# Kernel tuning notes

Measured on AMD Instinct MI355X. Metric: run time of the kernel, lower is better.

Reference implementation:

```python
import jax, jax.numpy as jnp
import numpy as np

# ---- config (mirrors init_kwargs) ----
H = 128
W = 128
FMO_STEPS = 4
INPUT_FRAMES = 1
N_PIECES = 1
N_TERMS = 2
CAM_DIST = 2.0
ROT_DIVIDE = 1.0
SIGMAINV = 7000.0
ERODE_K = 5
FOCAL = float(1.0 / np.tan(1.57 / 4.0))  # generate_perspective_projection(1.57/2), aspect=1


def quaternion_to_angle_axis(q):
    # q: [B,4] in (w,x,y,z) convention (torchgeometry)
    q1, q2, q3 = q[..., 1], q[..., 2], q[..., 3]
    sin_sq = q1 * q1 + q2 * q2 + q3 * q3
    sin_t = jnp.sqrt(sin_sq + 1e-20)
    cos_t = q[..., 0]
    two_theta = 2.0 * jnp.where(cos_t < 0.0, jnp.arctan2(-sin_t, -cos_t), jnp.arctan2(sin_t, cos_t))
    k = jnp.where(sin_sq > 1e-12, two_theta / sin_t, 2.0)
    return q[..., 1:4] * k[..., None]


def angle_axis_to_rotation_matrix(aa):
    # aa: [B,3] -> [B,3,3] (Rodrigues)
    th = jnp.sqrt(jnp.sum(aa * aa, axis=-1, keepdims=True) + 1e-12)  # [B,1]
    k = aa / th
    kx, ky, kz = k[..., 0], k[..., 1], k[..., 2]
    zero = jnp.zeros_like(kx)
    K = jnp.stack([jnp.stack([zero, -kz, ky], -1),
                   jnp.stack([kz, zero, -kx], -1),
                   jnp.stack([-ky, kx, zero], -1)], -2)
    s = jnp.sin(th)[..., None]
    c = jnp.cos(th)[..., None]
    return jnp.eye(3, dtype=aa.dtype) + s * K + (1.0 - c) * jnp.matmul(K, K)


def rasterize(fv_img, fv_z, face_feat, fn_z):
    # fv_img [B,F,3,2] NDC, fv_z [B,F,3] camera z, face_feat [B,F,3,C], fn_z [B,F]
    B, F = fv_img.shape[:2]
    xs = jnp.linspace(-1.0, 1.0, W)
    ys = jnp.linspace(1.0, -1.0, H)
    py, px = jnp.meshgrid(ys, xs, indexing='ij')  # [H,W]
    a, b, c = fv_img[:, :, 0], fv_img[:, :, 1], fv_img[:, :, 2]  # [B,F,2]
    e0 = b - a
    e1 = c - a
    denom = e0[..., 0] * e1[..., 1] - e0[..., 1] * e1[..., 0]  # [B,F]
    valid = (fn_z > 0.0) & (jnp.abs(denom) > 1e-10)
    inv_den = jnp.where(jnp.abs(denom) > 1e-10, 1.0 / denom, 0.0)
    dx = px[None, None] - a[..., 0][..., None, None]  # [B,F,H,W]
    dy = py[None, None] - a[..., 1][..., None, None]
    w1 = (dx * e1[..., 1][..., None, None] - dy * e1[..., 0][..., None, None]) * inv_den[..., None, None]
    w2 = (e0[..., 0][..., None, None] * dy - e0[..., 1][..., None, None] * dx) * inv_den[..., None, None]
    w0 = 1.0 - w1 - w2
    inside = (w0 >= 0.0) & (w1 >= 0.0) & (w2 >= 0.0) & valid[..., None, None]
    zi = (w0 * fv_z[:, :, 0, None, None] + w1 * fv_z[:, :, 1, None, None] + w2 * fv_z[:, :, 2, None, None])
    score = jnp.where(inside, zi, -1e10)  # camera looks down -z: nearest face has max z
    best = jnp.argmax(score, axis=1)      # [B,H,W] z-buffer winner
    hit = jnp.any(inside, axis=1)
    bary = jnp.stack([w0, w1, w2], axis=-1)  # [B,F,H,W,3]
    idx = jnp.broadcast_to(best[:, None, :, :, None], (B, 1, H, W, 3))
    bary_b = jnp.take_along_axis(bary, idx, axis=1)[:, 0]  # [B,H,W,3]
    feat_b = jax.vmap(lambda f, i: f[i])(face_feat, best)  # [B,H,W,3,C]
    feats = jnp.einsum('bhwkc,bhwk->bhwc', feat_b, bary_b) * hit[..., None]
    # DIB-R soft silhouette: A = 1 - prod(1 - exp(-sigmainv*d^2)), d = dist to triangle, 0 inside
    d2 = None
    tri = (a, b, c)
    for i in range(3):
        p, q = tri[i], tri[(i + 1) % 3]
        ex = (q - p)[..., 0][..., None, None]
        ey = (q - p)[..., 1][..., None, None]
        rx = px[None, None] - p[..., 0][..., None, None]
        ry = py[None, None] - p[..., 1][..., None, None]
        L2 = ex * ex + ey * ey + 1e-12
        t = jnp.clip((rx * ex + ry * ey) / L2, 0.0, 1.0)
        dxe = rx - t * ex
        dye = ry - t * ey
        dd = dxe * dxe + dye * dye
        d2 = dd if d2 is None else jnp.minimum(d2, dd)
    d2 = jnp.where(inside, 0.0, d2)
    prob = jnp.where(valid[..., None, None], jnp.exp(-SIGMAINV * d2), 0.0)
    mask = 1.0 - jnp.prod(1.0 - prob, axis=1)  # [B,H,W]
    return feats, mask


def texture_sample(tex, uv):
    # tex [B,3,Th,Tw], uv [B,H,W,2] in [0,1]; bilinear, v axis flipped (image row 0 <-> v=1)
    Th, Tw = tex.shape[2], tex.shape[3]
    u = jnp.clip(uv[..., 0], 0.0, 1.0) * (Tw - 1)
    v = (1.0 - jnp.clip(uv[..., 1], 0.0, 1.0)) * (Th - 1)
    x0 = jnp.floor(u)
    y0 = jnp.floor(v)
    fx = (u - x0)[:, None]  # [B,1,H,W]
    fy = (v - y0)[:, None]
    x0i = jnp.clip(x0.astype(jnp.int32), 0, Tw - 1)
    x1i = jnp.clip(x0i + 1, 0, Tw - 1)
    y0i = jnp.clip(y0.astype(jnp.int32), 0, Th - 1)
    y1i = jnp.clip(y0i + 1, 0, Th - 1)
    g = jax.vmap(lambda t, yy, xx: t[:, yy, xx])  # [B,3,H,W]
    t00 = g(tex, y0i, x0i)
    t01 = g(tex, y0i, x1i)
    t10 = g(tex, y1i, x0i)
    t11 = g(tex, y1i, x1i)
    return t00 * (1 - fx) * (1 - fy) + t01 * fx * (1 - fy) + t10 * (1 - fx) * fy + t11 * fx * fy


def erode(m, k):
    # kornia erosion with an all-ones kxk kernel == min-pool (geodesic border)
    return -jax.lax.reduce_window(-m, -jnp.inf, jax.lax.max, (1, k, k), (1, 1, 1), 'SAME')


def render_frame(verts_world, faces, face_features, texture_maps):
    # camera at (0,0,CAM_DIST) looking at origin with up=(0,1,0): R_cam == I
    v_cam = verts_world - jnp.array([0.0, 0.0, CAM_DIST], dtype=verts_world.dtype)
    fv_cam = v_cam[:, faces]  # [B,F,3,3]
    n = jnp.cross(fv_cam[:, :, 1] - fv_cam[:, :, 0], fv_cam[:, :, 2] - fv_cam[:, :, 0])
    n = n / (jnp.linalg.norm(n, axis=-1, keepdims=True) + 1e-10)
    fn_z = n[..., 2]
    z = fv_cam[..., 2]  # negative in front of camera
    img = FOCAL * fv_cam[..., :2] / (-z[..., None] + 1e-10)  # [B,F,3,2]
    uv, mask = rasterize(img, z, face_features, fn_z)
    rgb = texture_sample(texture_maps, uv)  # [B,3,H,W]
    mask_e = erode(mask, ERODE_K)
    return jnp.concatenate([rgb, mask_e[:, None]], axis=1)  # [B,4,H,W]


def reference(vertices, translation, quaternion, exp, face_features, texture_maps, faces):
    rot = angle_axis_to_rotation_matrix(quaternion_to_angle_axis(quaternion[:, 0, 0]))
    trans_start = translation[:, :, 0, 0]  # [B,1,3]
    all_renders = []
    renders = []
    frames = 0
    time_before = 0.0
    for pind in range(N_PIECES):
        angles = quaternion_to_angle_axis(quaternion[:, pind, 1]) / ROT_DIVIDE
        rot_step = angle_axis_to_rotation_matrix(exp * angles / FMO_STEPS)
        rot_noexp = angle_axis_to_rotation_matrix(angles * (1.0 - exp))
        n_steps = FMO_STEPS * INPUT_FRAMES // N_PIECES  # prop[pind] (forced for single piece)
        for ti in np.linspace(0.0, 1.0, n_steps):
            if frames == 0:
                time_before = ti
            time_exp = time_before + (ti - time_before) * exp  # [1]
            verts = jnp.einsum('bij,bvj->bvi', rot, vertices) + trans_start
            for p in range(1, N_TERMS):
                verts = verts + (time_exp ** p) * translation[:, :, pind, p]
            renders.append(render_frame(verts, faces, face_features, texture_maps))
            frames += 1
            if frames == FMO_STEPS:
                frames = 0
                all_renders.append(jnp.stack(renders, 1))
                renders = []
                rot = jnp.matmul(rot, rot_noexp)
            else:
                rot = jnp.matmul(rot, rot_step)
        for p in range(1, N_TERMS):
            trans_start = trans_start + translation[:, :, pind, p]
    return jnp.stack(all_renders, 1)  # [B, input_frames, fmo_steps, 4, H, W]


def setup_inputs() -> dict:
    key = jax.random.key(0)
    ks = jax.random.split(key, 7)
    B, V, F = 1, 162, 320
    vertices = jax.random.normal(ks[0], (B, V, 3), jnp.float32) * 0.3
    translation = jax.random.normal(ks[1], (B, 1, N_PIECES, N_TERMS, 3), jnp.float32) * 0.1
    quaternion = jax.random.normal(ks[2], (B, N_PIECES, 2, 4), jnp.float32)
    exp = jax.random.uniform(ks[3], (1,), jnp.float32)
    face_features = jax.random.uniform(ks[4], (B, F, 3, 2), jnp.float32)
    texture_maps = jax.random.uniform(ks[5], (B, 3, 256, 256), jnp.float32)
    faces = jax.random.randint(ks[6], (F, 3), 0, V)
    return {"vertices": vertices, "translation": translation, "quaternion": quaternion,
            "exp": exp, "face_features": face_features, "texture_maps": texture_maps,
            "faces": faces}
```

## Files before the change

### kernel.cpp

```cpp
#include <hip/hip_runtime.h>
#include <math.h>

#define N_FRAMES 4
#define N_FACES  320
#define N_VERTS  162
#define IMG_H    128
#define IMG_W    128
#define NWAVES   8
#define FPW      40
#define REC_SZ   20

#define SV_OFF   0
#define BB_OFF   1952
#define BB_LD    48
#define REC_OFF  8096
#define ARENA_SZ 33696



__device__ __forceinline__ void q_to_aa(const float* q, float* aa) {
    float q1 = q[1], q2 = q[2], q3 = q[3];
    float sin_sq = (q1 * q1 + q2 * q2) + q3 * q3;
    float sin_t = sqrtf(sin_sq + 1e-20f);
    float cos_t = q[0];
    float two_theta = (cos_t < 0.0f) ? (2.0f * atan2f(-sin_t, -cos_t))
                                     : (2.0f * atan2f(sin_t, cos_t));
    float k = (sin_sq > 1e-12f) ? (two_theta / sin_t) : 2.0f;
    aa[0] = q1 * k; aa[1] = q2 * k; aa[2] = q3 * k;
}

__device__ __forceinline__ void aa_to_R(const float* aa, float* R) {
    float th = sqrtf(((aa[0] * aa[0] + aa[1] * aa[1]) + aa[2] * aa[2]) + 1e-12f);
    float kx = aa[0] / th, ky = aa[1] / th, kz = aa[2] / th;
    float K[9] = { 0.0f, -kz,  ky,
                   kz,  0.0f, -kx,
                  -ky,   kx, 0.0f };
    float s = sinf(th), c = cosf(th);
    float KK[9];
    for (int i = 0; i < 3; ++i)
        for (int j = 0; j < 3; ++j)
            KK[i*3+j] = (K[i*3+0] * K[0*3+j] + K[i*3+1] * K[1*3+j]) + K[i*3+2] * K[2*3+j];
    float omc = 1.0f - c;
    for (int i = 0; i < 9; ++i) {
        float eye = (i == 0 || i == 4 || i == 8) ? 1.0f : 0.0f;
        R[i] = (eye + s * K[i]) + omc * KK[i];
    }
}

__device__ __forceinline__ void mat3mul(const float* A, const float* B, float* C) {
    for (int i = 0; i < 3; ++i)
        for (int j = 0; j < 3; ++j)
            C[i*3+j] = (A[i*3+0] * B[0*3+j] + A[i*3+1] * B[1*3+j]) + A[i*3+2] * B[2*3+j];
}


__global__ void __launch_bounds__(512)
render_kernel(const float* __restrict__ verts_in,
              const float* __restrict__ transl,
              const float* __restrict__ quat,
              const float* __restrict__ expv,
              const int*   __restrict__ faces,
              const float* __restrict__ ffeat,
              const float* __restrict__ tex,
              float* __restrict__ out,
              float* __restrict__ maskbuf)
{
    __shared__ __align__(16) char arena[ARENA_SZ];
    __shared__ float rotS[9];
    float* sv   = (float*)(arena + SV_OFF);
    float* bb   = (float*)(arena + BB_OFF);
    float* recs = (float*)(arena + REC_OFF);
    float* red  = (float*)arena;

    int frame = blockIdx.x >> 8;
    int blk   = blockIdx.x & 255;
    int tid   = threadIdx.x;
    int lane  = tid & 63;
    int wv    = __builtin_amdgcn_readfirstlane(tid >> 6);
    int tile_x = blk & 7, tile_y = blk >> 3;
    int j = tile_x * 16 + (lane & 15);
    int i = tile_y * 4 + (lane >> 4);

    float e = expv[0];

    if (tid == 0) {
        float aa0[3], aa1[3], Rl[9], S[9];
        q_to_aa(quat, aa0);
        aa_to_R(aa0, Rl);
        q_to_aa(quat + 4, aa1);
        float arg[3];
        for (int t = 0; t < 3; ++t) arg[t] = (e * aa1[t]) / 4.0f;
        aa_to_R(arg, S);
        for (int t = 0; t < frame; ++t) {
            float nxt[9];
            mat3mul(Rl, S, nxt);
            for (int q = 0; q < 9; ++q) Rl[q] = nxt[q];
        }
        for (int q = 0; q < 9; ++q) rotS[q] = Rl[q];
    }
    __syncthreads();

    if (tid < N_VERTS) {
        float te = (float)((double)frame / 3.0) * e;
        float vx = verts_in[tid*3+0], vy = verts_in[tid*3+1], vz = verts_in[tid*3+2];
        float dx_ = (rotS[0] * vx + rotS[1] * vy) + rotS[2] * vz;
        float dy_ = (rotS[3] * vx + rotS[4] * vy) + rotS[5] * vz;
        float dz_ = (rotS[6] * vx + rotS[7] * vy) + rotS[8] * vz;
        float x = (dx_ + transl[0]) + te * transl[3];
        float y = (dy_ + transl[1]) + te * transl[4];
        float z = (dz_ + transl[2]) + te * transl[5];
        z = z - 2.0f;
        sv[tid*3+0] = x; sv[tid*3+1] = y; sv[tid*3+2] = z;
    }
    __syncthreads();

    const float FOCAL = (float)(1.0 / tan(1.57 / 4.0));
    int cnt;
    {
        bool valid = false;
        float ax=0, ay=0, bx=0, by=0, cx=0, cy=0, e0x=0, e0y=0, e1x=0, e1y=0;
        float e12x=0, e12y=0, z0=0, z1=0, z2=0, den=0;
        int f = wv * FPW + lane;
        if (lane < FPW) {
            int i0 = faces[f*3+0], i1 = faces[f*3+1], i2 = faces[f*3+2];
            const float* A = &sv[i0*3];
            const float* B = &sv[i1*3];
            const float* C = &sv[i2*3];
            float ux = B[0] - A[0], uy = B[1] - A[1];
            float wx = C[0] - A[0], wy = C[1] - A[1];
            float nz = ux * wy - uy * wx;
            float da = -A[2] + 1e-10f, db = -B[2] + 1e-10f, dc = -C[2] + 1e-10f;
            ax = (FOCAL * A[0]) / da; ay = (FOCAL * A[1]) / da;
            bx = (FOCAL * B[0]) / db; by = (FOCAL * B[1]) / db;
            cx = (FOCAL * C[0]) / dc; cy = (FOCAL * C[1]) / dc;
            e0x = bx - ax; e0y = by - ay;
            e1x = cx - ax; e1y = cy - ay;
            e12x = cx - bx; e12y = cy - by;
            den = e0x * e1y - e0y * e1x;
            z0 = A[2]; z1 = B[2]; z2 = C[2];
            valid = (fabsf(den) > 1e-10f) && (nz > 0.0f);
        }
        unsigned long long m = __ballot(valid);
        cnt = __popcll(m);
        if (valid) {
            unsigned long long lmask = (lane == 63) ? 0x7fffffffffffffffull
                                                    : ((1ull << lane) - 1ull);
            int pos = __popcll(m & lmask);
            float invden = 1.0f / den;
            float L2_0 = (e0x * e0x + e0y * e0y) + 1e-12f;
            float L2_1 = (e12x * e12x + e12y * e12y) + 1e-12f;
            float L2_2 = (e1x * e1x + e1y * e1y) + 1e-12f;
            float4* r = (float4*)&recs[(wv * FPW + pos) * REC_SZ];
            r[0] = make_float4(ax, ay, e0x, e0y);
            r[1] = make_float4(e1x, e1y, invden, (float)f);
            r[2] = make_float4(z0, z1, z2, 1.0f / L2_0);
            r[3] = make_float4(bx, by, e12x, e12y);
            r[4] = make_float4(cx, cy, 1.0f / L2_1, 1.0f / L2_2);
            float* wbb = &bb[wv * 4 * BB_LD];
            wbb[0*BB_LD + pos] = fminf(fminf(ax, bx), cx);
            wbb[1*BB_LD + pos] = fminf(fminf(ay, by), cy);
            wbb[2*BB_LD + pos] = fmaxf(fmaxf(ax, bx), cx);
            wbb[3*BB_LD + pos] = fmaxf(fmaxf(ay, by), cy);
        }
    }

    float px = (float)(-1.0 + 2.0 * (double)j / 127.0);
    float py = (float)( 1.0 - 2.0 * (double)i / 127.0);
    float txmin = (float)(-1.0 + 2.0 * (double)(tile_x * 16) / 127.0);
    float txmax = (float)(-1.0 + 2.0 * (double)(tile_x * 16 + 15) / 127.0);
    float tymax = (float)( 1.0 - 2.0 * (double)(tile_y * 4) / 127.0);
    float tymin = (float)( 1.0 - 2.0 * (double)(tile_y * 4 + 3) / 127.0);

    unsigned long long fmask;
    {
        int l = (lane < FPW) ? lane : 0;
        const float* wbb = &bb[wv * 4 * BB_LD];
        float xmin = wbb[0*BB_LD + l], ymin = wbb[1*BB_LD + l];
        float xmax = wbb[2*BB_LD + l], ymax = wbb[3*BB_LD + l];
        float cdx = fmaxf(fmaxf(xmin - txmax, txmin - xmax), 0.0f);
        float cdy = fmaxf(fmaxf(ymin - tymax, tymin - ymax), 0.0f);
        bool near = ((cdx * cdx + cdy * cdy) <= 0.0026f) && (lane < cnt);
        fmask = __ballot(near);
    }

    float best = -1e10f;
    int bestf = 0;
    float bw0 = 0.0f, bw1 = 0.0f, bw2 = 0.0f;
    float P = 1.0f;
    bool pzero = false;

    while (fmask) {
        int fc = __ffsll((unsigned long long)fmask) - 1;
        fmask &= fmask - 1;
        const float* d = &recs[(wv * FPW + fc) * REC_SZ];

        float ax = d[0], ay = d[1], e0x = d[2], e0y = d[3];
        float e1x = d[4], e1y = d[5], invden = d[6], fidx = d[7];
        float z0 = d[8], z1 = d[9], z2 = d[10];

        float dx = px - ax, dy = py - ay;
        float w1 = (dx * e1y - dy * e1x) * invden;
        float w2 = (e0x * dy - e0y * dx) * invden;
        float w0 = (1.0f - w1) - w2;
        bool inside = (w0 >= 0.0f) & (w1 >= 0.0f) & (w2 >= 0.0f);
        float zi = (w0 * z0 + w1 * z1) + w2 * z2;
        float score = inside ? zi : -1e10f;
        if (score > best) {
            best = score; bestf = (int)fidx; bw0 = w0; bw1 = w1; bw2 = w2;
        }

        if (!pzero) {
            float invL2_0 = d[11];
            float bx = d[12], by = d[13], e12x = d[14], e12y = d[15];
            float cx = d[16], cy = d[17], invL2_1 = d[18], invL2_2 = d[19];
            float t0 = fminf(fmaxf((dx * e0x + dy * e0y) * invL2_0, 0.0f), 1.0f);
            float x0 = dx - t0 * e0x, y0 = dy - t0 * e0y;
            float dd = x0 * x0 + y0 * y0;
            float rx1 = px - bx, ry1 = py - by;
            float t1 = fminf(fmaxf((rx1 * e12x + ry1 * e12y) * invL2_1, 0.0f), 1.0f);
            float x1 = rx1 - t1 * e12x, y1 = ry1 - t1 * e12y;
            dd = fminf(dd, x1 * x1 + y1 * y1);
            float ex2 = -e1x, ey2 = -e1y;
            float rx2 = px - cx, ry2 = py - cy;
            float t2 = fminf(fmaxf((rx2 * ex2 + ry2 * ey2) * invL2_2, 0.0f), 1.0f);
            float x2 = rx2 - t2 * ex2, y2 = ry2 - t2 * ey2;
            dd = fminf(dd, x2 * x2 + y2 * y2);

            float d2 = inside ? 0.0f : dd;
            float prob = __expf(-7000.0f * d2);
            P *= (1.0f - prob);
            pzero = __all(P == 0.0f);
        }
    }

    __syncthreads();
    float* my = &red[tid * 6];
    my[0] = best; my[1] = __int_as_float(bestf);
    my[2] = bw0;  my[3] = bw1; my[4] = bw2; my[5] = P;
    __syncthreads();

    if (tid < 64) {
        float bbst = red[tid * 6 + 0];
        int   bf   = __float_as_int(red[tid * 6 + 1]);
        float r0 = red[tid * 6 + 2], r1 = red[tid * 6 + 3], r2 = red[tid * 6 + 4];
        float Pt = red[tid * 6 + 5];
        for (int w = 1; w < NWAVES; ++w) {
            const float* s = &red[(w * 64 + tid) * 6];
            float sc = s[0]; int ff = __float_as_int(s[1]);
            if ((sc > bbst) || ((sc == bbst) && (ff < bf))) {
                bbst = sc; bf = ff; r0 = s[2]; r1 = s[3]; r2 = s[4];
            }
            Pt *= s[5];
        }

        bool hit = bbst != -1e10f;
        float uv0 = 0.0f, uv1 = 0.0f;
        if (hit) {
            const float* fp = ffeat + bf * 6;
            uv0 = (fp[0] * r0 + fp[2] * r1) + fp[4] * r2;
            uv1 = (fp[1] * r0 + fp[3] * r1) + fp[5] * r2;
        }
        float u = fminf(fmaxf(uv0, 0.0f), 1.0f) * 255.0f;
        float v = (1.0f - fminf(fmaxf(uv1, 0.0f), 1.0f)) * 255.0f;
        float x0f = floorf(u), y0f = floorf(v);
        float fx = u - x0f, fy = v - y0f;
        int x0i = min(max((int)x0f, 0), 255);
        int x1i = min(x0i + 1, 255);
        int y0i = min(max((int)y0f, 0), 255);
        int y1i = min(y0i + 1, 255);

        for (int c = 0; c < 3; ++c) {
            const float* tc = tex + c * 65536;
            float t00 = tc[y0i * 256 + x0i];
            float t01 = tc[y0i * 256 + x1i];
            float t10 = tc[y1i * 256 + x0i];
            float t11 = tc[y1i * 256 + x1i];
            float val = (t00 * (1.0f - fx)) * (1.0f - fy);
            val = val + (t01 * fx) * (1.0f - fy);
            val = val + (t10 * (1.0f - fx)) * fy;
            val = val + (t11 * fx) * fy;
            out[((frame * 4 + c) * IMG_H + i) * IMG_W + j] = val;
        }
        maskbuf[(frame * IMG_H + i) * IMG_W + j] = 1.0f - Pt;
    }
}


__global__ void __launch_bounds__(256)
erode_kernel(const float* __restrict__ maskbuf, float* __restrict__ out)
{
    int frame = blockIdx.x >> 6;
    int pix = (blockIdx.x & 63) * 256 + threadIdx.x;
    int i = pix >> 7, j = pix & 127;
    float m = 1e30f;
    for (int di = -2; di <= 2; ++di) {
        int ii = i + di;
        if (ii < 0 || ii >= IMG_H) continue;
        for (int dj = -2; dj <= 2; ++dj) {
            int jj = j + dj;
            if (jj < 0 || jj >= IMG_W) continue;
            m = fminf(m, maskbuf[(frame * IMG_H + ii) * IMG_W + jj]);
        }
    }
    out[((frame * 4 + 3) * IMG_H + i) * IMG_W + j] = m;
}


extern "C" void kernel_launch(void* const* d_in, const int* in_sizes, int n_in,
                              void* d_out, int out_size, void* d_ws, size_t ws_size,
                              hipStream_t stream) {
    const float* vertices      = (const float*)d_in[0];
    const float* translation   = (const float*)d_in[1];
    const float* quaternion    = (const float*)d_in[2];
    const float* expv          = (const float*)d_in[3];
    const float* face_features = (const float*)d_in[4];
    const float* texture_maps  = (const float*)d_in[5];
    const int*   faces         = (const int*)d_in[6];
    float* out = (float*)d_out;

    float* maskbuf = (float*)d_ws;

    render_kernel<<<N_FRAMES * 256, 512, 0, stream>>>(vertices, translation,
                                                      quaternion, expv, faces,
                                                      face_features, texture_maps,
                                                      out, maskbuf);
    erode_kernel<<<N_FRAMES * 64, 256, 0, stream>>>(maskbuf, out);
}
```

Baseline: 87.94 us.

## Fuse erosion into render kernel by recomputing halo mask pixels per tile

Removes the separate erode kernel and its global mask buffer round trip. Each tile now evaluates the soft mask probability for a 2-pixel halo (96 extra pixels), with the face culling bounds widened to cover the halo. The block then performs the 5x5 min erosion from shared memory. This saves a kernel launch and global traffic, but adds redundant halo computation across 96 extra pixels per 64-pixel tile.

```diff
diff --git a/kernel.cpp b/kernel.cpp
--- a/kernel.cpp
+++ b/kernel.cpp
@@ -53,6 +53,42 @@
             C[i*3+j] = (A[i*3+0] * B[0*3+j] + A[i*3+1] * B[1*3+j]) + A[i*3+2] * B[2*3+j];
 }
 
+__device__ __forceinline__ void halo_rc(int h, int* r, int* c) {
+    if (h < 40)      { *r = h / 20;                *c = h % 20; }
+    else if (h < 80) { int idx = h - 40; *r = 6 + idx / 20; *c = idx % 20; }
+    else             { int s = h - 80; *r = 2 + (s >> 2);
+                       int co = s & 3; *c = (co < 2) ? co : (16 + co); }
+}
+
+__device__ __forceinline__ float face_mask_factor(
+    float px, float py,
+    float ax, float ay, float e0x, float e0y, float e1x, float e1y,
+    float invden, float invL2_0,
+    float bx, float by, float e12x, float e12y,
+    float cx, float cy, float invL2_1, float invL2_2)
+{
+    float dx = px - ax, dy = py - ay;
+    float w1 = (dx * e1y - dy * e1x) * invden;
+    float w2 = (e0x * dy - e0y * dx) * invden;
+    float w0 = (1.0f - w1) - w2;
+    bool inside = (w0 >= 0.0f) & (w1 >= 0.0f) & (w2 >= 0.0f);
+    float t0 = fminf(fmaxf((dx * e0x + dy * e0y) * invL2_0, 0.0f), 1.0f);
+    float x0 = dx - t0 * e0x, y0 = dy - t0 * e0y;
+    float dd = x0 * x0 + y0 * y0;
+    float rx1 = px - bx, ry1 = py - by;
+    float t1 = fminf(fmaxf((rx1 * e12x + ry1 * e12y) * invL2_1, 0.0f), 1.0f);
+    float x1 = rx1 - t1 * e12x, y1 = ry1 - t1 * e12y;
+    dd = fminf(dd, x1 * x1 + y1 * y1);
+    float ex2 = -e1x, ey2 = -e1y;
+    float rx2 = px - cx, ry2 = py - cy;
+    float t2 = fminf(fmaxf((rx2 * ex2 + ry2 * ey2) * invL2_2, 0.0f), 1.0f);
+    float x2 = rx2 - t2 * ex2, y2 = ry2 - t2 * ey2;
+    dd = fminf(dd, x2 * x2 + y2 * y2);
+    float d2 = inside ? 0.0f : dd;
+    float prob = __expf(-7000.0f * d2);
+    return 1.0f - prob;
+}
+
 
 __global__ void __launch_bounds__(512)
 render_kernel(const float* __restrict__ verts_in,
@@ -62,15 +98,16 @@
               const int*   __restrict__ faces,
               const float* __restrict__ ffeat,
               const float* __restrict__ tex,
-              float* __restrict__ out,
-              float* __restrict__ maskbuf)
+              float* __restrict__ out)
 {
     __shared__ __align__(16) char arena[ARENA_SZ];
     __shared__ float rotS[9];
-    float* sv   = (float*)(arena + SV_OFF);
-    float* bb   = (float*)(arena + BB_OFF);
-    float* recs = (float*)(arena + REC_OFF);
-    float* red  = (float*)arena;
+    float* sv    = (float*)(arena + SV_OFF);
+    float* bb    = (float*)(arena + BB_OFF);
+    float* recs  = (float*)(arena + REC_OFF);
+    float* red   = (float*)arena;
+    float* hredp = (float*)(arena + 12288);
+    float* m20   = (float*)(arena + 15360);
 
     int frame = blockIdx.x >> 8;
     int blk   = blockIdx.x & 255;
@@ -166,10 +203,10 @@
 
     float px = (float)(-1.0 + 2.0 * (double)j / 127.0);
     float py = (float)( 1.0 - 2.0 * (double)i / 127.0);
-    float txmin = (float)(-1.0 + 2.0 * (double)(tile_x * 16) / 127.0);
-    float txmax = (float)(-1.0 + 2.0 * (double)(tile_x * 16 + 15) / 127.0);
-    float tymax = (float)( 1.0 - 2.0 * (double)(tile_y * 4) / 127.0);
-    float tymin = (float)( 1.0 - 2.0 * (double)(tile_y * 4 + 3) / 127.0);
+    float txminH = (float)(-1.0 + 2.0 * (double)(tile_x * 16 - 2) / 127.0);
+    float txmaxH = (float)(-1.0 + 2.0 * (double)(tile_x * 16 + 17) / 127.0);
+    float tymaxH = (float)( 1.0 - 2.0 * (double)(tile_y * 4 - 2) / 127.0);
+    float tyminH = (float)( 1.0 - 2.0 * (double)(tile_y * 4 + 5) / 127.0);
 
     unsigned long long fmask;
     {
@@ -177,11 +214,12 @@
         const float* wbb = &bb[wv * 4 * BB_LD];
         float xmin = wbb[0*BB_LD + l], ymin = wbb[1*BB_LD + l];
         float xmax = wbb[2*BB_LD + l], ymax = wbb[3*BB_LD + l];
-        float cdx = fmaxf(fmaxf(xmin - txmax, txmin - xmax), 0.0f);
-        float cdy = fmaxf(fmaxf(ymin - tymax, tymin - ymax), 0.0f);
+        float cdx = fmaxf(fmaxf(xmin - txmaxH, txminH - xmax), 0.0f);
+        float cdy = fmaxf(fmaxf(ymin - tymaxH, tyminH - ymax), 0.0f);
         bool near = ((cdx * cdx + cdy * cdy) <= 0.0026f) && (lane < cnt);
         fmask = __ballot(near);
     }
+    unsigned long long fmask_h = fmask;
 
     float best = -1e10f;
     int bestf = 0;
@@ -233,10 +271,48 @@
         }
     }
 
+    float PA = 1.0f, PB = 0.0f;
+    {
+        int rA, cA; halo_rc(lane, &rA, &cA);
+        int iA = tile_y * 4 + rA - 2, jA = tile_x * 16 + cA - 2;
+        float pxA = (float)(-1.0 + 2.0 * (double)jA / 127.0);
+        float pyA = (float)( 1.0 - 2.0 * (double)iA / 127.0);
+        bool hasB = lane < 32;
+        float pxB = pxA, pyB = pyA;
+        if (hasB) {
+            int rB, cB; halo_rc(64 + lane, &rB, &cB);
+            int iB = tile_y * 4 + rB - 2, jB = tile_x * 16 + cB - 2;
+            pxB = (float)(-1.0 + 2.0 * (double)jB / 127.0);
+            pyB = (float)( 1.0 - 2.0 * (double)iB / 127.0);
+            PB = 1.0f;
+        }
+        bool hzero = false;
+        while (fmask_h && !hzero) {
+            int fc = __ffsll((unsigned long long)fmask_h) - 1;
+            fmask_h &= fmask_h - 1;
+            const float* d = &recs[(wv * FPW + fc) * REC_SZ];
+            float ax = d[0], ay = d[1], e0x = d[2], e0y = d[3];
+            float e1x = d[4], e1y = d[5], invden = d[6];
+            float invL2_0 = d[11];
+            float bx = d[12], by = d[13], e12x = d[14], e12y = d[15];
+            float cx = d[16], cy = d[17], invL2_1 = d[18], invL2_2 = d[19];
+            PA *= face_mask_factor(pxA, pyA, ax, ay, e0x, e0y, e1x, e1y,
+                                   invden, invL2_0, bx, by, e12x, e12y,
+                                   cx, cy, invL2_1, invL2_2);
+            if (hasB)
+                PB *= face_mask_factor(pxB, pyB, ax, ay, e0x, e0y, e1x, e1y,
+                                       invden, invL2_0, bx, by, e12x, e12y,
+                                       cx, cy, invL2_1, invL2_2);
+            hzero = __all((PA == 0.0f) & (PB == 0.0f));
+        }
+    }
+
     __syncthreads();
     float* my = &red[tid * 6];
     my[0] = best; my[1] = __int_as_float(bestf);
     my[2] = bw0;  my[3] = bw1; my[4] = bw2; my[5] = P;
+    hredp[wv * 96 + lane] = PA;
+    if (lane < 32) hredp[wv * 96 + 64 + lane] = PB;
     __syncthreads();
 
     if (tid < 64) {
@@ -281,28 +357,26 @@
             val = val + (t11 * fx) * fy;
             out[((frame * 4 + c) * IMG_H + i) * IMG_W + j] = val;
         }
-        maskbuf[(frame * IMG_H + i) * IMG_W + j] = 1.0f - Pt;
-    }
-}
-
-
-__global__ void __launch_bounds__(256)
-erode_kernel(const float* __restrict__ maskbuf, float* __restrict__ out)
-{
-    int frame = blockIdx.x >> 6;
-    int pix = (blockIdx.x & 63) * 256 + threadIdx.x;
-    int i = pix >> 7, j = pix & 127;
-    float m = 1e30f;
-    for (int di = -2; di <= 2; ++di) {
-        int ii = i + di;
-        if (ii < 0 || ii >= IMG_H) continue;
-        for (int dj = -2; dj <= 2; ++dj) {
-            int jj = j + dj;
-            if (jj < 0 || jj >= IMG_W) continue;
-            m = fminf(m, maskbuf[(frame * IMG_H + ii) * IMG_W + jj]);
-        }
-    }
-    out[((frame * 4 + 3) * IMG_H + i) * IMG_W + j] = m;
+        m20[(2 + (tid >> 4)) * 20 + (2 + (tid & 15))] = 1.0f - Pt;
+    } else if (tid < 160) {
+        int h = tid - 64;
+        float p = hredp[h];
+        for (int w = 1; w < NWAVES; ++w) p *= hredp[w * 96 + h];
+        int r, c; halo_rc(h, &r, &c);
+        int ii = tile_y * 4 + r - 2, jj = tile_x * 16 + c - 2;
+        bool inimg = (ii >= 0) && (ii < IMG_H) && (jj >= 0) && (jj < IMG_W);
+        m20[r * 20 + c] = inimg ? (1.0f - p) : 1e30f;
+    }
+    __syncthreads();
+
+    if (tid < 64) {
+        int r = 2 + (tid >> 4), c = 2 + (tid & 15);
+        float mn = 1e30f;
+        for (int dr = -2; dr <= 2; ++dr)
+            for (int dc = -2; dc <= 2; ++dc)
+                mn = fminf(mn, m20[(r + dr) * 20 + (c + dc)]);
+        out[((frame * 4 + 3) * IMG_H + i) * IMG_W + j] = mn;
+    }
 }
 
 
@@ -317,12 +391,10 @@
     const float* texture_maps  = (const float*)d_in[5];
     const int*   faces         = (const int*)d_in[6];
     float* out = (float*)d_out;
-
-    float* maskbuf = (float*)d_ws;
+    (void)d_ws; (void)ws_size;
 
     render_kernel<<<N_FRAMES * 256, 512, 0, stream>>>(vertices, translation,
                                                       quaternion, expv, faces,
                                                       face_features, texture_maps,
-                                                      out, maskbuf);
-    erode_kernel<<<N_FRAMES * 64, 256, 0, stream>>>(maskbuf, out);
-}
+                                                      out);
+}
```

Result: slower. 103.4 us (+17.6%).
